# Kernel tuning notes

Hardware: AMD Instinct MI355X
Metric: run time of the kernel (lower is better)

Reference implementation:

```python
import jax, jax.numpy as jnp
import numpy as np

EPS = 1e-5
NUM_HEADS = 12

def _ln(x, g, b):
    m = jnp.mean(x, -1, keepdims=True)
    v = jnp.var(x, -1, keepdims=True)
    return (x - m) * jax.lax.rsqrt(v + EPS) * g + b

def setup_inputs():
    key = jax.random.key(0)
    ks = jax.random.split(key, 8)
    D, Dh = 768, 3072
    B, T, H, Wd = 8, 8, 14, 14
    def w(k, shape, scale=0.02):
        return jax.random.normal(k, shape, jnp.float32) * scale
    return dict(
        x=jax.random.normal(ks[0], (B, T * H * Wd + 1, D), jnp.float32),
        W_mq=w(ks[1], (D, D)), b_mq=jnp.zeros((D,), jnp.float32),
        W_mk=w(ks[2], (D, D)), b_mk=jnp.zeros((D,), jnp.float32),
        g1=jnp.ones((D,), jnp.float32), be1=jnp.zeros((D,), jnp.float32),
        W_qkv=w(ks[3], (3 * D, D)),
        W_proj=w(ks[4], (D, D)), b_proj=jnp.zeros((D,), jnp.float32),
        g2=jnp.ones((D,), jnp.float32), be2=jnp.zeros((D,), jnp.float32),
        W_fc1=w(ks[5], (Dh, D)), b_fc1=jnp.zeros((Dh,), jnp.float32),
        W_fc2=w(ks[6], (D, Dh)), b_fc2=jnp.zeros((D,), jnp.float32),
        B=B, T=T, H=H, Wd=Wd,
    )

def reference(x, W_mq, b_mq, W_mk, b_mk, g1, be1, W_qkv, W_proj, b_proj,
              g2, be2, W_fc1, b_fc1, W_fc2, b_fc2, B, T, H, Wd):
    D = x.shape[-1]
    nh = NUM_HEADS
    hd = D // nh
    res = x
    # cls token: (B,1,D) -> repeated per frame -> (B*T,1,D)
    cls = jnp.repeat(x[:, :1, :], T, axis=1).reshape(B * T, 1, D)
    # spatial tokens: 'b (h w t) m -> (b t) (h w) m'  (t is fastest-varying)
    xs = x[:, 1:, :].reshape(B, H * Wd, T, D).transpose(0, 2, 1, 3).reshape(B * T, H * Wd, D)
    xt = jnp.concatenate([cls, xs], axis=1)  # (BT, N=197, D)
    # learned QK-gated mask
    qm = xt @ W_mq.T + b_mq
    km = xt @ W_mk.T + b_mk
    lm = jnp.einsum('bnd,bmd->bnm', qm, km)
    lm = lm.at[:, 0, 0].set(100.0)  # force cls->cls gate open
    lm = jax.nn.sigmoid(lm)
    # attention (drop rates are 0; drop_path is identity at inference)
    xn = _ln(xt, g1, be1)
    BT, N = xt.shape[0], xt.shape[1]
    qkv = (xn @ W_qkv.T).reshape(BT, N, 3, nh, hd).transpose(2, 0, 3, 1, 4)
    q, k, v = qkv[0], qkv[1], qkv[2]  # (BT, nh, N, hd)
    attn = jax.nn.softmax(jnp.einsum('bhnd,bhmd->bhnm', q, k) * (hd ** -0.5), axis=-1)
    attn = attn * lm[:, None, :, :]  # gate attention probs with learned mask
    o = jnp.einsum('bhnm,bhmd->bhnd', attn, v).transpose(0, 2, 1, 3).reshape(BT, N, D)
    o = o @ W_proj.T + b_proj
    # gather cls back (mean over frames) and scatter tokens back
    cls_o = jnp.mean(o[:, 0, :].reshape(B, T, D), axis=1, keepdims=True)  # (B,1,D)
    xs_o = o[:, 1:, :].reshape(B, T, H * Wd, D).transpose(0, 2, 1, 3).reshape(B, H * Wd * T, D)
    y = res + jnp.concatenate([cls_o, xs_o], axis=1)
    # MLP
    h = _ln(y, g2, be2)
    h = jax.nn.gelu(h @ W_fc1.T + b_fc1, approximate=False)
    y = y + (h @ W_fc2.T + b_fc2)
    return (y, lm)
```

## Files before the change

### kernel.cpp

```cpp
#include <hip/hip_runtime.h>
#include <cstdint>

typedef _Float16 f16;
typedef f16 f16x2 __attribute__((ext_vector_type(2)));
typedef f16 f16x4 __attribute__((ext_vector_type(4)));
typedef f16 f16x8 __attribute__((ext_vector_type(8)));
typedef float f32x4 __attribute__((ext_vector_type(4)));

constexpr int D = 768;
constexpr int NTOK = 197;
constexpr int BT = 64;
constexpr int ROWS_A = BT * NTOK;
constexpr int SEQ = 1569;
constexpr int ROWS_Y = 8 * SEQ;
constexpr int DH = 3072;
constexpr int CW = 2304;
constexpr long Y_ELEMS = (long)ROWS_Y * D;
constexpr long LM_ELEMS = (long)BT * NTOK * NTOK;

__global__ __launch_bounds__(256) void cvt_f16(const float* __restrict__ in,
                                               f16* __restrict__ out, int n4) {
  int i = blockIdx.x * 256 + threadIdx.x;
  if (i >= n4) return;
  const float4 v = *(const float4*)(in + (size_t)i * 4);
  f16x4 o = {(f16)v.x, (f16)v.y, (f16)v.z, (f16)v.w};
  *(f16x4*)(out + (size_t)i * 4) = o;
}

__global__ __launch_bounds__(192) void build_xt_xn(
    const float* __restrict__ x, const float* __restrict__ g1,
    const float* __restrict__ be1, f16* __restrict__ xt, f16* __restrict__ xn) {
  const int rid = blockIdx.x;
  const int bt = rid / NTOK, n = rid % NTOK;
  const int b = bt >> 3, t = bt & 7;
  const int src = (n == 0) ? b * SEQ : b * SEQ + 1 + (n - 1) * 8 + t;
  const int tid = threadIdx.x, d0 = tid * 4;
  const float4 v = *(const float4*)(x + (size_t)src * D + d0);
  float s = v.x + v.y + v.z + v.w;
  float q = v.x * v.x + v.y * v.y + v.z * v.z + v.w * v.w;
  const int lane = tid & 63, wv = tid >> 6;
  for (int off = 32; off; off >>= 1) {
    s += __shfl_xor(s, off);
    q += __shfl_xor(q, off);
  }
  __shared__ float red[2][3];
  if (lane == 0) { red[0][wv] = s; red[1][wv] = q; }
  __syncthreads();
  s = red[0][0] + red[0][1] + red[0][2];
  q = red[1][0] + red[1][1] + red[1][2];
  const float mean = s * (1.f / 768.f);
  const float var = q * (1.f / 768.f) - mean * mean;
  const float rs = rsqrtf(var + 1e-5f);
  const size_t ob = (size_t)rid * D + d0;
  f16x4 xo = {(f16)v.x, (f16)v.y, (f16)v.z, (f16)v.w};
  *(f16x4*)(xt + ob) = xo;
  const float4 gv = *(const float4*)(g1 + d0);
  const float4 bv = *(const float4*)(be1 + d0);
  f16x4 no = {(f16)((v.x - mean) * rs * gv.x + bv.x),
              (f16)((v.y - mean) * rs * gv.y + bv.y),
              (f16)((v.z - mean) * rs * gv.z + bv.z),
              (f16)((v.w - mean) * rs * gv.w + bv.w)};
  *(f16x4*)(xn + ob) = no;
}

constexpr int EPI_F16 = 0;
constexpr int EPI_F16_BIAS = 1;
constexpr int EPI_SIG = 2;
constexpr int EPI_F16_BIAS_GELU = 3;
constexpr int EPI_F32_BIAS_RES = 4;

template <int EPI>
__global__ __launch_bounds__(256, 2) void gemm_f16(
    const f16* __restrict__ A, const f16* __restrict__ B,
    const float* __restrict__ bias, float* __restrict__ Cf,
    f16* __restrict__ Ch, const float* __restrict__ Res, int M, int N, int K,
    int ldc, long sA, long sB, long sC) {
  constexpr int BM = 128, BN = 128, BK = 32, PK = 40;
  __shared__ f16 As[BM][PK];
  __shared__ f16 Bs[BN][PK];
  const int tid = threadIdx.x;
  const int bm = blockIdx.y * BM, bn = blockIdx.x * BN;
  const int z = blockIdx.z;
  A += (size_t)z * sA;
  B += (size_t)z * sB;
  const int lane = tid & 63, wave = tid >> 6;
  const int wm = (wave >> 1) * 64, wn = (wave & 1) * 64;
  const int lr = lane & 15, lk = (lane >> 4) * 8;
  const int srow = tid >> 2, scol = (tid & 3) * 8;

  f32x4 acc[4][4] = {};

  for (int kt = 0; kt < K; kt += BK) {
#pragma unroll
    for (int i = 0; i < 2; i++) {
      const int r = srow + i * 64;
      const int gm = bm + r, gn = bn + r;
      f16x8 av = {}, bv = {};
      if (gm < M) av = *(const f16x8*)(A + (size_t)gm * K + kt + scol);
      if (gn < N) bv = *(const f16x8*)(B + (size_t)gn * K + kt + scol);
      *(f16x8*)&As[r][scol] = av;
      *(f16x8*)&Bs[r][scol] = bv;
    }
    __syncthreads();
    f16x8 af[4], bf[4];
#pragma unroll
    for (int i = 0; i < 4; i++) {
      af[i] = *(const f16x8*)&As[wm + i * 16 + lr][lk];
      bf[i] = *(const f16x8*)&Bs[wn + i * 16 + lr][lk];
    }
#pragma unroll
    for (int i = 0; i < 4; i++)
#pragma unroll
      for (int j = 0; j < 4; j++)
        acc[i][j] =
            __builtin_amdgcn_mfma_f32_16x16x32_f16(af[i], bf[j], acc[i][j], 0, 0, 0);
    __syncthreads();
  }

#pragma unroll
  for (int i = 0; i < 4; i++) {
#pragma unroll
    for (int j = 0; j < 4; j++) {
      const int col = bn + wn + j * 16 + lr;
      if (col >= N) continue;
#pragma unroll
      for (int r = 0; r < 4; r++) {
        const int row = bm + wm + i * 16 + (lane >> 4) * 4 + r;
        if (row >= M) continue;
        float v = acc[i][j][r];
        const size_t ci = (size_t)z * sC + (size_t)row * ldc + col;
        if constexpr (EPI == EPI_F16) {
          Ch[ci] = (f16)v;
        } else if constexpr (EPI == EPI_F16_BIAS) {
          Ch[ci] = (f16)(v + bias[col]);
        } else if constexpr (EPI == EPI_SIG) {
          if (row == 0 && col == 0) v = 100.f;
          Cf[ci] = 1.f / (1.f + __expf(-v));
        } else if constexpr (EPI == EPI_F16_BIAS_GELU) {
          v += bias[col];
          Ch[ci] = (f16)(0.5f * v * (1.f + erff(v * 0.70710678118f)));
        } else if constexpr (EPI == EPI_F32_BIAS_RES) {
          Cf[ci] = v + bias[col] + Res[ci];
        }
      }
    }
  }
}

__global__ __launch_bounds__(256, 2) void attn_kernel(
    const f16* __restrict__ qkv, const float* __restrict__ lm,
    f16* __restrict__ o) {
  __shared__ f16 Ks[208][72];
  __shared__ f16 Vt[64][232];
  __shared__ f16 Ps[4][16][40];
  const int bh = blockIdx.x;
  const int bt = bh / 12, h = bh % 12;
  const int tid = threadIdx.x, lane = tid & 63, w = tid >> 6;
  const int l15 = lane & 15, quad = lane >> 4;
  const size_t base = (size_t)bt * NTOK * CW + (size_t)h * 64;

  for (int idx = tid; idx < 208 * 8; idx += 256) {
    const int r = idx >> 3, c = (idx & 7) * 8;
    f16x8 kv = {};
    if (r < NTOK) kv = *(const f16x8*)(qkv + base + (size_t)r * CW + 768 + c);
    *(f16x8*)&Ks[r][c] = kv;
  }
  for (int cb = 0; cb < 8; cb++) {
    const int r = tid;
    if (r < NTOK) {
      const f16x8 vv = *(const f16x8*)(qkv + base + (size_t)r * CW + 1536 + cb * 8);
#pragma unroll
      for (int j = 0; j < 8; j++) Vt[cb * 8 + j][r] = vv[j];
    }
  }
  for (int idx = tid; idx < 64 * 35; idx += 256) {
    const int d = idx / 35, m = NTOK + idx % 35;
    Vt[d][m] = (f16)0.f;
  }
  __syncthreads();

  for (int nt = w; nt < 13; nt += 4) {
    const int nq = nt * 16 + l15;
    const f16* qrow = qkv + base + (size_t)nq * CW;
    const f16x8 aq0 = *(const f16x8*)(qrow + quad * 8);
    const f16x8 aq1 = *(const f16x8*)(qrow + 32 + quad * 8);
    f32x4 S[13];
#pragma unroll
    for (int t = 0; t < 13; t++) {
      const f16x8 bk0 = *(const f16x8*)&Ks[t * 16 + l15][quad * 8];
      const f16x8 bk1 = *(const f16x8*)&Ks[t * 16 + l15][32 + quad * 8];
      f32x4 s = {};
      s = __builtin_amdgcn_mfma_f32_16x16x32_f16(aq0, bk0, s, 0, 0, 0);
      s = __builtin_amdgcn_mfma_f32_16x16x32_f16(aq1, bk1, s, 0, 0, 0);
      S[t] = s;
    }
    float mx[4] = {-3e38f, -3e38f, -3e38f, -3e38f};
#pragma unroll
    for (int t = 0; t < 13; t++) {
      const int m = t * 16 + l15;
#pragma unroll
      for (int r = 0; r < 4; r++) {
        float v = (m < NTOK) ? S[t][r] * 0.125f : -1e30f;
        S[t][r] = v;
        mx[r] = fmaxf(mx[r], v);
      }
    }
#pragma unroll
    for (int off = 1; off < 16; off <<= 1)
#pragma unroll
      for (int r = 0; r < 4; r++) mx[r] = fmaxf(mx[r], __shfl_xor(mx[r], off));
    float den[4] = {0.f, 0.f, 0.f, 0.f};
#pragma unroll
    for (int t = 0; t < 13; t++)
#pragma unroll
      for (int r = 0; r < 4; r++) {
        const float e = __expf(S[t][r] - mx[r]);
        S[t][r] = e;
        den[r] += e;
      }
#pragma unroll
    for (int off = 1; off < 16; off <<= 1)
#pragma unroll
      for (int r = 0; r < 4; r++) den[r] += __shfl_xor(den[r], off);
    float inv[4];
#pragma unroll
    for (int r = 0; r < 4; r++) inv[r] = 1.f / den[r];
#pragma unroll
    for (int t = 0; t < 13; t++) {
      const int m = t * 16 + l15;
#pragma unroll
      for (int r = 0; r < 4; r++) {
        const int nrow = nt * 16 + quad * 4 + r;
        float g = 0.f;
        if (m < NTOK && nrow < NTOK)
          g = lm[((size_t)bt * NTOK + nrow) * NTOK + m];
        S[t][r] *= inv[r] * g;
      }
    }
    f32x4 O[4] = {};
    for (int c = 0; c < 7; c++) {
      __builtin_amdgcn_wave_barrier();
#pragma unroll
      for (int tt = 0; tt < 2; tt++) {
        const int t = 2 * c + tt;
#pragma unroll
        for (int r = 0; r < 4; r++) {
          const f16 pv = (t < 13) ? (f16)S[t][r] : (f16)0.f;
          Ps[w][quad * 4 + r][tt * 16 + l15] = pv;
        }
      }
      __builtin_amdgcn_wave_barrier();
      const f16x8 ap = *(const f16x8*)&Ps[w][l15][quad * 8];
#pragma unroll
      for (int dt = 0; dt < 4; dt++) {
        const f16x8 bv = *(const f16x8*)&Vt[dt * 16 + l15][c * 32 + quad * 8];
        O[dt] = __builtin_amdgcn_mfma_f32_16x16x32_f16(ap, bv, O[dt], 0, 0, 0);
      }
    }
#pragma unroll
    for (int dt = 0; dt < 4; dt++)
#pragma unroll
      for (int r = 0; r < 4; r++) {
        const int nrow = nt * 16 + quad * 4 + r;
        if (nrow < NTOK)
          o[((size_t)bt * NTOK + nrow) * D + h * 64 + dt * 16 + l15] =
              (f16)O[dt][r];
      }
  }
}

__global__ __launch_bounds__(192) void scatter_y_ln(
    const float* __restrict__ x, const f16* __restrict__ po,
    const float* __restrict__ g2, const float* __restrict__ be2,
    float* __restrict__ y, f16* __restrict__ yn) {
  const int rid = blockIdx.x;
  const int b = rid / SEQ, pos = rid % SEQ;
  const int tid = threadIdx.x, d0 = tid * 4;
  float4 v = *(const float4*)(x + (size_t)rid * D + d0);
  if (pos == 0) {
    float ax = 0, ay = 0, az = 0, aw = 0;
    for (int t = 0; t < 8; t++) {
      const f16x4 p = *(const f16x4*)(po + ((size_t)(b * 8 + t) * NTOK) * D + d0);
      ax += (float)p[0]; ay += (float)p[1]; az += (float)p[2]; aw += (float)p[3];
    }
    v.x += ax * 0.125f; v.y += ay * 0.125f; v.z += az * 0.125f; v.w += aw * 0.125f;
  } else {
    const int hw = (pos - 1) >> 3, t = (pos - 1) & 7;
    const f16x4 p =
        *(const f16x4*)(po + ((size_t)((b * 8 + t) * NTOK + 1 + hw)) * D + d0);
    v.x += (float)p[0]; v.y += (float)p[1]; v.z += (float)p[2]; v.w += (float)p[3];
  }
  *(float4*)(y + (size_t)rid * D + d0) = v;
  float s = v.x + v.y + v.z + v.w;
  float q = v.x * v.x + v.y * v.y + v.z * v.z + v.w * v.w;
  const int lane = tid & 63, wv = tid >> 6;
  for (int off = 32; off; off >>= 1) {
    s += __shfl_xor(s, off);
    q += __shfl_xor(q, off);
  }
  __shared__ float red[2][3];
  if (lane == 0) { red[0][wv] = s; red[1][wv] = q; }
  __syncthreads();
  s = red[0][0] + red[0][1] + red[0][2];
  q = red[1][0] + red[1][1] + red[1][2];
  const float mean = s * (1.f / 768.f);
  const float var = q * (1.f / 768.f) - mean * mean;
  const float rs = rsqrtf(var + 1e-5f);
  const float4 gv = *(const float4*)(g2 + d0);
  const float4 bv = *(const float4*)(be2 + d0);
  f16x4 no = {(f16)((v.x - mean) * rs * gv.x + bv.x),
              (f16)((v.y - mean) * rs * gv.y + bv.y),
              (f16)((v.z - mean) * rs * gv.z + bv.z),
              (f16)((v.w - mean) * rs * gv.w + bv.w)};
  *(f16x4*)(yn + (size_t)rid * D + d0) = no;
}

extern "C" void kernel_launch(void* const* d_in, const int* in_sizes, int n_in,
                              void* d_out, int out_size, void* d_ws,
                              size_t ws_size, hipStream_t stream) {
  const float* x = (const float*)d_in[0];
  const float* W_mq = (const float*)d_in[1];
  const float* b_mq = (const float*)d_in[2];
  const float* W_mk = (const float*)d_in[3];
  const float* b_mk = (const float*)d_in[4];
  const float* g1 = (const float*)d_in[5];
  const float* be1 = (const float*)d_in[6];
  const float* W_qkv = (const float*)d_in[7];
  const float* W_proj = (const float*)d_in[8];
  const float* b_proj = (const float*)d_in[9];
  const float* g2 = (const float*)d_in[10];
  const float* be2 = (const float*)d_in[11];
  const float* W_fc1 = (const float*)d_in[12];
  const float* b_fc1 = (const float*)d_in[13];
  const float* W_fc2 = (const float*)d_in[14];
  const float* b_fc2 = (const float*)d_in[15];

  char* ws = (char*)d_ws;
  size_t off = 0;
  auto alloc = [&](size_t bytes) {
    size_t o = off;
    off = (off + bytes + 255) & ~(size_t)255;
    return o;
  };
  const size_t o_wmq = alloc((size_t)D * D * 2);
  const size_t o_wmk = alloc((size_t)D * D * 2);
  const size_t o_wqkv = alloc((size_t)CW * D * 2);
  const size_t o_wproj = alloc((size_t)D * D * 2);
  const size_t o_wfc1 = alloc((size_t)DH * D * 2);
  const size_t o_wfc2 = alloc((size_t)D * DH * 2);
  const size_t o_xt = alloc((size_t)ROWS_A * D * 2);
  const size_t o_xn = alloc((size_t)ROWS_A * D * 2);
  const size_t o_qm = alloc((size_t)ROWS_A * D * 2);
  alloc((size_t)ROWS_A * D * 2);
  const size_t o_km = o_qm + (size_t)ROWS_A * D * 2;
  const size_t o_qkv = o_qm;
  const size_t o_o = o_xn;
  const size_t o_po = o_qm + (size_t)ROWS_A * CW * 2;
  const size_t o_yn = o_xt;
  const size_t o_h = o_qm;

  f16* wmq = (f16*)(ws + o_wmq);
  f16* wmk = (f16*)(ws + o_wmk);
  f16* wqkv = (f16*)(ws + o_wqkv);
  f16* wproj = (f16*)(ws + o_wproj);
  f16* wfc1 = (f16*)(ws + o_wfc1);
  f16* wfc2 = (f16*)(ws + o_wfc2);
  f16* xt = (f16*)(ws + o_xt);
  f16* xn = (f16*)(ws + o_xn);
  f16* qm = (f16*)(ws + o_qm);
  f16* km = (f16*)(ws + o_km);
  f16* qkv = (f16*)(ws + o_qkv);
  f16* oatt = (f16*)(ws + o_o);
  f16* po = (f16*)(ws + o_po);
  f16* yn = (f16*)(ws + o_yn);
  f16* h = (f16*)(ws + o_h);

  float* y_out = (float*)d_out;
  float* lm_out = (float*)d_out + Y_ELEMS;

  const dim3 blk(256);
  auto cvt = [&](const float* src, f16* dst, int n) {
    cvt_f16<<<dim3((n / 4 + 255) / 256), blk, 0, stream>>>(src, dst, n / 4);
  };
  cvt(W_mq, wmq, D * D);
  cvt(W_mk, wmk, D * D);
  cvt(W_qkv, wqkv, CW * D);
  cvt(W_proj, wproj, D * D);
  cvt(W_fc1, wfc1, DH * D);
  cvt(W_fc2, wfc2, D * DH);

  build_xt_xn<<<dim3(ROWS_A), dim3(192), 0, stream>>>(x, g1, be1, xt, xn);

  auto grd = [](int N_, int M_, int Z_) {
    return dim3((N_ + 127) / 128, (M_ + 127) / 128, Z_);
  };
  gemm_f16<EPI_F16_BIAS><<<grd(D, ROWS_A, 1), blk, 0, stream>>>(
      xt, wmq, b_mq, nullptr, qm, nullptr, ROWS_A, D, D, D, 0, 0, 0);
  gemm_f16<EPI_F16_BIAS><<<grd(D, ROWS_A, 1), blk, 0, stream>>>(
      xt, wmk, b_mk, nullptr, km, nullptr, ROWS_A, D, D, D, 0, 0, 0);
  gemm_f16<EPI_SIG><<<grd(NTOK, NTOK, BT), blk, 0, stream>>>(
      qm, km, nullptr, lm_out, nullptr, nullptr, NTOK, NTOK, D, NTOK,
      (long)NTOK * D, (long)NTOK * D, (long)NTOK * NTOK);
  gemm_f16<EPI_F16><<<grd(CW, ROWS_A, 1), blk, 0, stream>>>(
      xn, wqkv, nullptr, nullptr, qkv, nullptr, ROWS_A, CW, D, CW, 0, 0, 0);
  attn_kernel<<<dim3(BT * 12), blk, 0, stream>>>(qkv, lm_out, oatt);
  gemm_f16<EPI_F16_BIAS><<<grd(D, ROWS_A, 1), blk, 0, stream>>>(
      oatt, wproj, b_proj, nullptr, po, nullptr, ROWS_A, D, D, D, 0, 0, 0);
  scatter_y_ln<<<dim3(ROWS_Y), dim3(192), 0, stream>>>(x, po, g2, be2, y_out, yn);
  gemm_f16<EPI_F16_BIAS_GELU><<<grd(DH, ROWS_Y, 1), blk, 0, stream>>>(
      yn, wfc1, b_fc1, nullptr, h, nullptr, ROWS_Y, DH, D, DH, 0, 0, 0);
  gemm_f16<EPI_F32_BIAS_RES><<<grd(D, ROWS_Y, 1), blk, 0, stream>>>(
      h, wfc2, b_fc2, y_out, nullptr, y_out, ROWS_Y, D, DH, D, 0, 0, 0);
  (void)in_sizes; (void)n_in; (void)out_size; (void)ws_size;
}
```

Measured before the change: 731.3 us.

## Load GEMM tiles directly into LDS with global_load_lds and raise occupancy

The f16 GEMM now copies its A and B tiles from global memory straight into shared memory using the buffer-to-LDS builtin, instead of loading into registers and then storing to LDS. Rows outside the matrix are clamped to the last valid row rather than zero-filled, since their results are never written. The LDS padding is dropped because the direct-load layout needs contiguous rows, and the launch bound is raised to request three blocks per CU. The aim is to cut register pressure and the extra instructions of the register staging step. In exchange, the unpadded 64-byte rows may cause LDS bank conflicts when fragments are read, and the loop is still single-buffered.

```diff
diff --git a/kernel.cpp b/kernel.cpp
--- a/kernel.cpp
+++ b/kernel.cpp
@@ -17,6 +17,12 @@
 constexpr int CW = 2304;
 constexpr long Y_ELEMS = (long)ROWS_Y * D;
 constexpr long LM_ELEMS = (long)BT * NTOK * NTOK;
+
+__device__ __forceinline__ void gload_lds16(const f16* g, f16* l) {
+  __builtin_amdgcn_global_load_lds(
+      (const __attribute__((address_space(1))) void*)g,
+      (__attribute__((address_space(3))) void*)l, 16, 0, 0);
+}
 
 __global__ __launch_bounds__(256) void cvt_f16(const float* __restrict__ in,
                                                f16* __restrict__ out, int n4) {
@@ -70,14 +76,14 @@
 constexpr int EPI_F32_BIAS_RES = 4;
 
 template <int EPI>
-__global__ __launch_bounds__(256, 2) void gemm_f16(
+__global__ __launch_bounds__(256, 3) void gemm_f16(
     const f16* __restrict__ A, const f16* __restrict__ B,
     const float* __restrict__ bias, float* __restrict__ Cf,
     f16* __restrict__ Ch, const float* __restrict__ Res, int M, int N, int K,
     int ldc, long sA, long sB, long sC) {
-  constexpr int BM = 128, BN = 128, BK = 32, PK = 40;
-  __shared__ f16 As[BM][PK];
-  __shared__ f16 Bs[BN][PK];
+  constexpr int BM = 128, BN = 128, BK = 32;
+  __shared__ f16 As[BM][BK];
+  __shared__ f16 Bs[BN][BK];
   const int tid = threadIdx.x;
   const int bm = blockIdx.y * BM, bn = blockIdx.x * BN;
   const int z = blockIdx.z;
@@ -85,28 +91,36 @@
   B += (size_t)z * sB;
   const int lane = tid & 63, wave = tid >> 6;
   const int wm = (wave >> 1) * 64, wn = (wave & 1) * 64;
-  const int lr = lane & 15, lk = (lane >> 4) * 8;
-  const int srow = tid >> 2, scol = (tid & 3) * 8;
+  const int l15 = lane & 15, quad = lane >> 4;
+
+  const int gr = lane >> 2;
+  const int gc = (lane & 3) * 8;
+  int a_row0 = bm + wave * 16 + gr;       if (a_row0 >= M) a_row0 = M - 1;
+  int a_row1 = bm + (wave + 4) * 16 + gr; if (a_row1 >= M) a_row1 = M - 1;
+  int b_row0 = bn + wave * 16 + gr;       if (b_row0 >= N) b_row0 = N - 1;
+  int b_row1 = bn + (wave + 4) * 16 + gr; if (b_row1 >= N) b_row1 = N - 1;
+  const f16* ap0 = A + (size_t)a_row0 * K + gc;
+  const f16* ap1 = A + (size_t)a_row1 * K + gc;
+  const f16* bp0 = B + (size_t)b_row0 * K + gc;
+  const f16* bp1 = B + (size_t)b_row1 * K + gc;
+  f16* as0 = &As[wave * 16][0];
+  f16* as1 = &As[(wave + 4) * 16][0];
+  f16* bs0 = &Bs[wave * 16][0];
+  f16* bs1 = &Bs[(wave + 4) * 16][0];
 
   f32x4 acc[4][4] = {};
 
   for (int kt = 0; kt < K; kt += BK) {
-#pragma unroll
-    for (int i = 0; i < 2; i++) {
-      const int r = srow + i * 64;
-      const int gm = bm + r, gn = bn + r;
-      f16x8 av = {}, bv = {};
-      if (gm < M) av = *(const f16x8*)(A + (size_t)gm * K + kt + scol);
-      if (gn < N) bv = *(const f16x8*)(B + (size_t)gn * K + kt + scol);
-      *(f16x8*)&As[r][scol] = av;
-      *(f16x8*)&Bs[r][scol] = bv;
-    }
+    gload_lds16(ap0 + kt, as0);
+    gload_lds16(ap1 + kt, as1);
+    gload_lds16(bp0 + kt, bs0);
+    gload_lds16(bp1 + kt, bs1);
     __syncthreads();
     f16x8 af[4], bf[4];
 #pragma unroll
     for (int i = 0; i < 4; i++) {
-      af[i] = *(const f16x8*)&As[wm + i * 16 + lr][lk];
-      bf[i] = *(const f16x8*)&Bs[wn + i * 16 + lr][lk];
+      af[i] = *(const f16x8*)&As[wm + i * 16 + l15][quad * 8];
+      bf[i] = *(const f16x8*)&Bs[wn + i * 16 + l15][quad * 8];
     }
 #pragma unroll
     for (int i = 0; i < 4; i++)
@@ -121,11 +135,11 @@
   for (int i = 0; i < 4; i++) {
 #pragma unroll
     for (int j = 0; j < 4; j++) {
-      const int col = bn + wn + j * 16 + lr;
+      const int col = bn + wn + j * 16 + l15;
       if (col >= N) continue;
 #pragma unroll
       for (int r = 0; r < 4; r++) {
-        const int row = bm + wm + i * 16 + (lane >> 4) * 4 + r;
+        const int row = bm + wm + i * 16 + quad * 4 + r;
         if (row >= M) continue;
         float v = acc[i][j][r];
         const size_t ci = (size_t)z * sC + (size_t)row * ldc + col;
```

After: 670.3 us. 8.3% less time.
